# Kernel optimization log

Hardware: AMD Instinct MI355X
Metric: run time of the kernel (lower is better)

Reference implementation:

```python
import jax, jax.numpy as jnp
import numpy as np

QMAX8 = 127.0  # 2**(8-1)-1


def quant1(x, scale):
    # 1-bit symmetric quant: s * sign(x), s = |scale| (per-group mean scale)
    return jnp.abs(scale) * jnp.sign(x)


def quant8(x, scale):
    s = jnp.maximum(jnp.abs(scale), 1e-8)
    q = jnp.clip(jnp.round(x / s), -QMAX8, QMAX8)
    return q * s


def setup_inputs() -> dict:
    key = jax.random.key(0)
    ks = jax.random.split(key, 5)
    p, j, k, m, l, n = 2, 32, 32, 32, 8, 32
    x = jax.random.normal(ks[0], (2, 1024, k * n), dtype=jnp.float32)
    Y_fp = jax.random.normal(ks[1], (p, j, k, m, l), dtype=jnp.float32)
    Z_fp = jax.random.normal(ks[2], (p, j, k, l, n), dtype=jnp.float32)
    A = jax.random.normal(ks[3], (p, j, k, 4), dtype=jnp.float32)
    bias = jax.random.normal(ks[4], (j * m,), dtype=jnp.float32)
    act_scale = jnp.full((1,), 0.001, dtype=jnp.float32)
    return {"x": x, "Y_fp": Y_fp, "Z_fp": Z_fp, "A": A, "bias": bias,
            "act_scale": act_scale}


def reference(x, Y_fp, Z_fp, A, bias, act_scale):
    p, j, k, m, l = Y_fp.shape
    n = Z_fp.shape[-1]
    orig_shape = x.shape[:-1]
    X = x.astype(jnp.float32)
    X = quant8(X, act_scale)  # activation quantization (act_bits=8)

    # per-(p,j,k) mean-abs scales over last two dims
    Y_scale = jnp.mean(jnp.abs(Y_fp), axis=(-2, -1), keepdims=True)
    Z_scale = jnp.mean(jnp.abs(Z_fp), axis=(-2, -1), keepdims=True)
    Y_q = quant1(Y_fp, Y_scale)  # (p,j,k,m,l)
    Z_q = quant1(Z_fp, Z_scale)  # (p,j,k,l,n)

    X_kn = X.reshape(-1, k, n)  # (B,k,n)
    T = jnp.einsum('bkn,pjkln->bpjkl', X_kn, Z_q)
    core = jnp.einsum('pjkml,bpjkl->bpjkm', Y_q, T)

    # quant_bias=True correction terms
    a = A[..., 0][None, ..., None]            # (1,p,j,k,1)
    out1 = jnp.sum(core * a, axis=(1, 3))     # (B,j,m)
    Y_sum = jnp.sum(Y_q, axis=-1)             # (p,j,k,m)
    B_coef = jnp.sum(A[..., 1][..., None] * Y_sum, axis=0)  # (j,k,m)
    Sx = jnp.sum(X_kn, axis=-1)               # (B,k)
    out2 = jnp.einsum('bk,jkm->bjm', Sx, B_coef)
    Zs = jnp.sum(Z_q, axis=-2)                # (p,j,k,n)
    Tz = jnp.einsum('bkn,pjkn->bpjk', X_kn, Zs)
    out3 = jnp.sum(Tz * A[..., 2][None], axis=(1, 3))[..., None]  # (B,j,1)
    D_coef = jnp.sum(A[..., 3], axis=0)       # (j,k)
    out4 = jnp.einsum('bk,jk->bj', Sx, D_coef)[..., None]          # (B,j,1)

    out_bjm = out1 + out2 + out3 + out4       # (B,j,m) via broadcast
    out_2d = out_bjm.reshape(-1, j * m) + bias
    out = out_2d.reshape(*orig_shape, j * m)
    return out.astype(x.dtype)
```

## Files before the change

kernel.cpp:

```cpp
#include <hip/hip_runtime.h>
#include <math.h>
#include <stdint.h>


typedef __attribute__((ext_vector_type(8))) short bf16x8;
typedef __attribute__((ext_vector_type(4))) float f32x4;
typedef __attribute__((ext_vector_type(4))) unsigned short us4;

__device__ __forceinline__ unsigned short f2bf(float f) {
    union { float f; uint32_t u; } c; c.f = f;
    uint32_t r = 0x7fffu + ((c.u >> 16) & 1u);
    return (unsigned short)((c.u + r) >> 16);
}

__device__ __forceinline__ void gl2lds16(const void* g, void* l) {
    __builtin_amdgcn_global_load_lds(
        (const __attribute__((address_space(1))) void*)g,
        (__attribute__((address_space(3))) void*)l, 16, 0, 0);
}

__global__ __launch_bounds__(256) void fused_pre(
    const float* __restrict__ Y,
    const float* __restrict__ Z,
    const float* __restrict__ A,
    const float* __restrict__ x,
    const float* __restrict__ act_scale,
    unsigned short* __restrict__ wt,
    unsigned short* __restrict__ qx)
{
    const int t = threadIdx.x;

    if (blockIdx.x >= 1024) {
        const float s = fmaxf(fabsf(act_scale[0]), 1e-8f);
        const int b2 = blockIdx.x - 1024;
        #pragma unroll
        for (int it = 0; it < 4; ++it) {
            const size_t i4 = (size_t)b2 * 256 + t + (size_t)it * 131072;
            const float4 v = *(const float4*)(x + i4 * 4);
            us4 o;
            o.x = f2bf(fminf(fmaxf(rintf(v.x / s), -127.f), 127.f));
            o.y = f2bf(fminf(fmaxf(rintf(v.y / s), -127.f), 127.f));
            o.z = f2bf(fminf(fmaxf(rintf(v.z / s), -127.f), 127.f));
            o.w = f2bf(fminf(fmaxf(rintf(v.w / s), -127.f), 127.f));
            *(us4*)(qx + i4 * 4) = o;
        }
        return;
    }

    __shared__ unsigned int yb[2][8];
    __shared__ unsigned int zb[2][8];
    __shared__ float wred[16];

    const int jk = blockIdx.x;
    const int jj = jk >> 5;
    const int kk = jk & 31;
    const int n  = t & 31;
    const int mb = t >> 5;
    const int w  = t >> 6;
    const int lane = t & 63;

    const int base0 = jj * 32 + kk;
    const int base1 = 1024 + base0;

    const float yv0 = Y[(size_t)base0 * 256 + t];
    const float yv1 = Y[(size_t)base1 * 256 + t];
    const float zv0 = Z[(size_t)base0 * 256 + t];
    const float zv1 = Z[(size_t)base1 * 256 + t];
    const float a00 = A[(size_t)base0 * 4 + 0], a01 = A[(size_t)base0 * 4 + 1];
    const float a02 = A[(size_t)base0 * 4 + 2], a03 = A[(size_t)base0 * 4 + 3];
    const float a10 = A[(size_t)base1 * 4 + 0], a11 = A[(size_t)base1 * 4 + 1];
    const float a12 = A[(size_t)base1 * 4 + 2], a13 = A[(size_t)base1 * 4 + 3];

    const unsigned long long by0 = __ballot(yv0 < 0.f);
    const unsigned long long by1 = __ballot(yv1 < 0.f);
    const unsigned long long bz0 = __ballot(zv0 < 0.f);
    const unsigned long long bz1 = __ballot(zv1 < 0.f);
    if (lane == 0) {
        yb[0][2 * w] = (unsigned)by0; yb[0][2 * w + 1] = (unsigned)(by0 >> 32);
        yb[1][2 * w] = (unsigned)by1; yb[1][2 * w + 1] = (unsigned)(by1 >> 32);
        zb[0][2 * w] = (unsigned)bz0; zb[0][2 * w + 1] = (unsigned)(bz0 >> 32);
        zb[1][2 * w] = (unsigned)bz1; zb[1][2 * w + 1] = (unsigned)(bz1 >> 32);
    }

    float ay0 = fabsf(yv0), az0 = fabsf(zv0);
    float ay1 = fabsf(yv1), az1 = fabsf(zv1);
    #pragma unroll
    for (int d = 1; d < 64; d <<= 1) {
        ay0 += __shfl_xor(ay0, d, 64);
        az0 += __shfl_xor(az0, d, 64);
        ay1 += __shfl_xor(ay1, d, 64);
        az1 += __shfl_xor(az1, d, 64);
    }
    if (lane == 0) {
        wred[w * 4 + 0] = ay0;
        wred[w * 4 + 1] = az0;
        wred[w * 4 + 2] = ay1;
        wred[w * 4 + 3] = az1;
    }
    __syncthreads();

    const float sY0 = (wred[0] + wred[4] + wred[8]  + wred[12]) * (1.f / 256.f);
    const float sZ0 = (wred[1] + wred[5] + wred[9]  + wred[13]) * (1.f / 256.f);
    const float sY1 = (wred[2] + wred[6] + wred[10] + wred[14]) * (1.f / 256.f);
    const float sZ1 = (wred[3] + wred[7] + wred[11] + wred[15]) * (1.f / 256.f);

    const float c00 = a00 * sY0 * sZ0, c01 = a01 * sY0, c02 = a02 * sZ0;
    const float c10 = a10 * sY1 * sZ1, c11 = a11 * sY1, c12 = a12 * sZ1;
    const float cb  = a03 + a13;

    unsigned sz0 = 0, sz1 = 0;
    #pragma unroll
    for (int l = 0; l < 8; ++l) {
        sz0 |= ((zb[0][l] >> n) & 1u) << l;
        sz1 |= ((zb[1][l] >> n) & 1u) << l;
    }
    const float zc0 = 8.f - 2.f * (float)__popc(sz0);
    const float zc1 = 8.f - 2.f * (float)__popc(sz1);
    const float czc = c02 * zc0 + c12 * zc1 + cb;

    const int ybw = (mb >> 2);
    const int ybs = (mb & 3) * 8;

    #pragma unroll
    for (int q = 0; q < 4; ++q) {
        const int m = mb + 8 * q;
        const unsigned sy0 = (yb[0][2 * q + ybw] >> ybs) & 0xffu;
        const unsigned sy1 = (yb[1][2 * q + ybw] >> ybs) & 0xffu;
        const float w0  = 8.f - 2.f * (float)__popc(sy0 ^ sz0);
        const float w1  = 8.f - 2.f * (float)__popc(sy1 ^ sz1);
        const float ys0 = 8.f - 2.f * (float)__popc(sy0);
        const float ys1 = 8.f - 2.f * (float)__popc(sy1);
        const float acc = c00 * w0 + c01 * ys0 + c10 * w1 + c11 * ys1 + czc;
        wt[(size_t)(jj * 32 + m) * 1024 + kk * 32 + n] = f2bf(acc);
    }
}

__global__ __launch_bounds__(256) void gemm_mfma(
    const unsigned short* __restrict__ qx,
    const unsigned short* __restrict__ wt,
    const float* __restrict__ bias,
    const float* __restrict__ act_scale,
    float* __restrict__ out)
{
    __shared__ __align__(16) short lds[2 * 16384];

    const int tid  = threadIdx.x;
    const int lane = tid & 63;
    const int wave = tid >> 6;
    const int wm = wave >> 1;
    const int wn = wave & 1;
    const int rowBase = blockIdx.y * 64;
    const int colBase = blockIdx.x * 64;

    const float s = fmaxf(fabsf(act_scale[0]), 1e-8f);

    f32x4 acc[2][2];
    #pragma unroll
    for (int i = 0; i < 2; ++i)
        #pragma unroll
        for (int jx = 0; jx < 2; ++jx)
            acc[i][jx] = (f32x4)0.f;

    const int lrow = lane >> 4;
    const int slot = lane & 15;
    const unsigned short* ag[4];
    const unsigned short* bg[4];
    #pragma unroll
    for (int is = 0; is < 4; ++is) {
        const int g   = is * 4 + wave;
        const int row = g * 4 + lrow;
        const int gk  = slot ^ (row & 15);
        ag[is] = qx + (size_t)(rowBase + row) * 1024 + gk * 8;
        bg[is] = wt + (size_t)(colBase + row) * 1024 + gk * 8;
    }

    char* const ldsc = (char*)lds;
    const int q4  = lane >> 4;
    const int l16 = lane & 15;

    #pragma unroll
    for (int is = 0; is < 4; ++is) {
        const int g = is * 4 + wave;
        gl2lds16(ag[is], ldsc + g * 1024);
        gl2lds16(bg[is], ldsc + 16384 + g * 1024);
    }

    for (int kt = 0; kt < 8; ++kt) {
        __syncthreads();

        if (kt + 1 < 8) {
            const int k1 = (kt + 1) * 128;
            char* bb = ldsc + ((kt + 1) & 1) * 32768;
            #pragma unroll
            for (int is = 0; is < 4; ++is) {
                const int g = is * 4 + wave;
                gl2lds16(ag[is] + k1, bb + g * 1024);
                gl2lds16(bg[is] + k1, bb + 16384 + g * 1024);
            }
        }

        const short* As = lds + (kt & 1) * 16384;
        const short* Bs = As + 8192;

        #pragma unroll
        for (int k2 = 0; k2 < 4; ++k2) {
            const int kc = k2 * 4 + q4;
            bf16x8 af[2], bfr[2];
            #pragma unroll
            for (int im = 0; im < 2; ++im) {
                const int r = wm * 32 + im * 16 + l16;
                af[im] = *(const bf16x8*)&As[r * 128 + ((kc ^ (r & 15)) << 3)];
            }
            #pragma unroll
            for (int in = 0; in < 2; ++in) {
                const int r = wn * 32 + in * 16 + l16;
                bfr[in] = *(const bf16x8*)&Bs[r * 128 + ((kc ^ (r & 15)) << 3)];
            }
            #pragma unroll
            for (int im = 0; im < 2; ++im)
                #pragma unroll
                for (int in = 0; in < 2; ++in)
                    acc[im][in] = __builtin_amdgcn_mfma_f32_16x16x32_bf16(
                        af[im], bfr[in], acc[im][in], 0, 0, 0);
        }
    }

    #pragma unroll
    for (int im = 0; im < 2; ++im) {
        #pragma unroll
        for (int in = 0; in < 2; ++in) {
            const int col = colBase + wn * 32 + in * 16 + l16;
            const float b = bias[col];
            #pragma unroll
            for (int r = 0; r < 4; ++r) {
                const int row = rowBase + wm * 32 + im * 16 + q4 * 4 + r;
                out[(size_t)row * 1024 + col] = s * acc[im][in][r] + b;
            }
        }
    }
}

extern "C" void kernel_launch(void* const* d_in, const int* in_sizes, int n_in,
                              void* d_out, int out_size, void* d_ws, size_t ws_size,
                              hipStream_t stream) {
    const float* x         = (const float*)d_in[0];
    const float* Y_fp      = (const float*)d_in[1];
    const float* Z_fp      = (const float*)d_in[2];
    const float* A         = (const float*)d_in[3];
    const float* bias      = (const float*)d_in[4];
    const float* act_scale = (const float*)d_in[5];
    float* out = (float*)d_out;

    unsigned short* wtp = (unsigned short*)d_ws;
    unsigned short* qxp = (unsigned short*)((char*)d_ws + 2 * 1024 * 1024);

    fused_pre<<<dim3(1536), dim3(256), 0, stream>>>(Y_fp, Z_fp, A, x, act_scale, wtp, qxp);
    gemm_mfma<<<dim3(16, 32), dim3(256), 0, stream>>>(qxp, wtp, bias, act_scale, out);
}
```

Before: 81.12 us.

## Fuse preprocessing and GEMM into one cooperative kernel with grid sync

```diff
diff --git a/kernel.cpp b/kernel.cpp
--- a/kernel.cpp
+++ b/kernel.cpp
@@ -1,6 +1,9 @@
 #include <hip/hip_runtime.h>
+#include <hip/hip_cooperative_groups.h>
 #include <math.h>
 #include <stdint.h>
+
+namespace cg = cooperative_groups;
 
 
 typedef __attribute__((ext_vector_type(8))) short bf16x8;
@@ -19,140 +22,149 @@
         (__attribute__((address_space(3))) void*)l, 16, 0, 0);
 }
 
-__global__ __launch_bounds__(256) void fused_pre(
+__global__ __launch_bounds__(256) void fused_all(
+    const float* __restrict__ x,
     const float* __restrict__ Y,
     const float* __restrict__ Z,
     const float* __restrict__ A,
-    const float* __restrict__ x,
+    const float* __restrict__ bias,
     const float* __restrict__ act_scale,
     unsigned short* __restrict__ wt,
-    unsigned short* __restrict__ qx)
-{
-    const int t = threadIdx.x;
-
-    if (blockIdx.x >= 1024) {
-        const float s = fmaxf(fabsf(act_scale[0]), 1e-8f);
-        const int b2 = blockIdx.x - 1024;
-        #pragma unroll
-        for (int it = 0; it < 4; ++it) {
-            const size_t i4 = (size_t)b2 * 256 + t + (size_t)it * 131072;
-            const float4 v = *(const float4*)(x + i4 * 4);
-            us4 o;
-            o.x = f2bf(fminf(fmaxf(rintf(v.x / s), -127.f), 127.f));
-            o.y = f2bf(fminf(fmaxf(rintf(v.y / s), -127.f), 127.f));
-            o.z = f2bf(fminf(fmaxf(rintf(v.z / s), -127.f), 127.f));
-            o.w = f2bf(fminf(fmaxf(rintf(v.w / s), -127.f), 127.f));
-            *(us4*)(qx + i4 * 4) = o;
-        }
-        return;
-    }
-
-    __shared__ unsigned int yb[2][8];
-    __shared__ unsigned int zb[2][8];
-    __shared__ float wred[16];
-
-    const int jk = blockIdx.x;
-    const int jj = jk >> 5;
-    const int kk = jk & 31;
-    const int n  = t & 31;
-    const int mb = t >> 5;
-    const int w  = t >> 6;
-    const int lane = t & 63;
-
-    const int base0 = jj * 32 + kk;
-    const int base1 = 1024 + base0;
-
-    const float yv0 = Y[(size_t)base0 * 256 + t];
-    const float yv1 = Y[(size_t)base1 * 256 + t];
-    const float zv0 = Z[(size_t)base0 * 256 + t];
-    const float zv1 = Z[(size_t)base1 * 256 + t];
-    const float a00 = A[(size_t)base0 * 4 + 0], a01 = A[(size_t)base0 * 4 + 1];
-    const float a02 = A[(size_t)base0 * 4 + 2], a03 = A[(size_t)base0 * 4 + 3];
-    const float a10 = A[(size_t)base1 * 4 + 0], a11 = A[(size_t)base1 * 4 + 1];
-    const float a12 = A[(size_t)base1 * 4 + 2], a13 = A[(size_t)base1 * 4 + 3];
-
-    const unsigned long long by0 = __ballot(yv0 < 0.f);
-    const unsigned long long by1 = __ballot(yv1 < 0.f);
-    const unsigned long long bz0 = __ballot(zv0 < 0.f);
-    const unsigned long long bz1 = __ballot(zv1 < 0.f);
-    if (lane == 0) {
-        yb[0][2 * w] = (unsigned)by0; yb[0][2 * w + 1] = (unsigned)(by0 >> 32);
-        yb[1][2 * w] = (unsigned)by1; yb[1][2 * w + 1] = (unsigned)(by1 >> 32);
-        zb[0][2 * w] = (unsigned)bz0; zb[0][2 * w + 1] = (unsigned)(bz0 >> 32);
-        zb[1][2 * w] = (unsigned)bz1; zb[1][2 * w + 1] = (unsigned)(bz1 >> 32);
-    }
-
-    float ay0 = fabsf(yv0), az0 = fabsf(zv0);
-    float ay1 = fabsf(yv1), az1 = fabsf(zv1);
-    #pragma unroll
-    for (int d = 1; d < 64; d <<= 1) {
-        ay0 += __shfl_xor(ay0, d, 64);
-        az0 += __shfl_xor(az0, d, 64);
-        ay1 += __shfl_xor(ay1, d, 64);
-        az1 += __shfl_xor(az1, d, 64);
-    }
-    if (lane == 0) {
-        wred[w * 4 + 0] = ay0;
-        wred[w * 4 + 1] = az0;
-        wred[w * 4 + 2] = ay1;
-        wred[w * 4 + 3] = az1;
-    }
-    __syncthreads();
-
-    const float sY0 = (wred[0] + wred[4] + wred[8]  + wred[12]) * (1.f / 256.f);
-    const float sZ0 = (wred[1] + wred[5] + wred[9]  + wred[13]) * (1.f / 256.f);
-    const float sY1 = (wred[2] + wred[6] + wred[10] + wred[14]) * (1.f / 256.f);
-    const float sZ1 = (wred[3] + wred[7] + wred[11] + wred[15]) * (1.f / 256.f);
-
-    const float c00 = a00 * sY0 * sZ0, c01 = a01 * sY0, c02 = a02 * sZ0;
-    const float c10 = a10 * sY1 * sZ1, c11 = a11 * sY1, c12 = a12 * sZ1;
-    const float cb  = a03 + a13;
-
-    unsigned sz0 = 0, sz1 = 0;
-    #pragma unroll
-    for (int l = 0; l < 8; ++l) {
-        sz0 |= ((zb[0][l] >> n) & 1u) << l;
-        sz1 |= ((zb[1][l] >> n) & 1u) << l;
-    }
-    const float zc0 = 8.f - 2.f * (float)__popc(sz0);
-    const float zc1 = 8.f - 2.f * (float)__popc(sz1);
-    const float czc = c02 * zc0 + c12 * zc1 + cb;
-
-    const int ybw = (mb >> 2);
-    const int ybs = (mb & 3) * 8;
-
-    #pragma unroll
-    for (int q = 0; q < 4; ++q) {
-        const int m = mb + 8 * q;
-        const unsigned sy0 = (yb[0][2 * q + ybw] >> ybs) & 0xffu;
-        const unsigned sy1 = (yb[1][2 * q + ybw] >> ybs) & 0xffu;
-        const float w0  = 8.f - 2.f * (float)__popc(sy0 ^ sz0);
-        const float w1  = 8.f - 2.f * (float)__popc(sy1 ^ sz1);
-        const float ys0 = 8.f - 2.f * (float)__popc(sy0);
-        const float ys1 = 8.f - 2.f * (float)__popc(sy1);
-        const float acc = c00 * w0 + c01 * ys0 + c10 * w1 + c11 * ys1 + czc;
-        wt[(size_t)(jj * 32 + m) * 1024 + kk * 32 + n] = f2bf(acc);
-    }
-}
-
-__global__ __launch_bounds__(256) void gemm_mfma(
-    const unsigned short* __restrict__ qx,
-    const unsigned short* __restrict__ wt,
-    const float* __restrict__ bias,
-    const float* __restrict__ act_scale,
+    unsigned short* __restrict__ qx,
     float* __restrict__ out)
 {
     __shared__ __align__(16) short lds[2 * 16384];
-
-    const int tid  = threadIdx.x;
-    const int lane = tid & 63;
-    const int wave = tid >> 6;
+    __shared__ unsigned int yb[2][2][8];
+    __shared__ unsigned int zb[2][2][8];
+    __shared__ float wred[2][16];
+
+    const int t    = threadIdx.x;
+    const int lane = t & 63;
+    const int w    = t >> 6;
+    const int bid  = blockIdx.y * 16 + blockIdx.x;
+
+    const float s = fmaxf(fabsf(act_scale[0]), 1e-8f);
+
+    float4 xq[4];
+    #pragma unroll
+    for (int it = 0; it < 4; ++it) {
+        const size_t i4 = (size_t)bid * 256 + t + (size_t)it * 131072;
+        xq[it] = *(const float4*)(x + i4 * 4);
+    }
+
+    const int n  = t & 31;
+    const int mb = t >> 5;
+
+    float yv[2][2], zv[2][2], ac[2][2][4];
+    int jjv[2], kkv[2];
+    #pragma unroll
+    for (int tt = 0; tt < 2; ++tt) {
+        const int jk = bid * 2 + tt;
+        jjv[tt] = jk >> 5;
+        kkv[tt] = jk & 31;
+        #pragma unroll
+        for (int p = 0; p < 2; ++p) {
+            const int base = p * 1024 + jjv[tt] * 32 + kkv[tt];
+            yv[tt][p] = Y[(size_t)base * 256 + t];
+            zv[tt][p] = Z[(size_t)base * 256 + t];
+            ac[tt][p][0] = A[(size_t)base * 4 + 0];
+            ac[tt][p][1] = A[(size_t)base * 4 + 1];
+            ac[tt][p][2] = A[(size_t)base * 4 + 2];
+            ac[tt][p][3] = A[(size_t)base * 4 + 3];
+        }
+    }
+
+    unsigned long long by[2][2], bz[2][2];
+    float ay[2][2], az[2][2];
+    #pragma unroll
+    for (int tt = 0; tt < 2; ++tt)
+        #pragma unroll
+        for (int p = 0; p < 2; ++p) {
+            by[tt][p] = __ballot(yv[tt][p] < 0.f);
+            bz[tt][p] = __ballot(zv[tt][p] < 0.f);
+            ay[tt][p] = fabsf(yv[tt][p]);
+            az[tt][p] = fabsf(zv[tt][p]);
+        }
+    #pragma unroll
+    for (int d = 1; d < 64; d <<= 1)
+        #pragma unroll
+        for (int tt = 0; tt < 2; ++tt)
+            #pragma unroll
+            for (int p = 0; p < 2; ++p) {
+                ay[tt][p] += __shfl_xor(ay[tt][p], d, 64);
+                az[tt][p] += __shfl_xor(az[tt][p], d, 64);
+            }
+    if (lane == 0) {
+        #pragma unroll
+        for (int tt = 0; tt < 2; ++tt)
+            #pragma unroll
+            for (int p = 0; p < 2; ++p) {
+                yb[tt][p][2 * w]     = (unsigned)by[tt][p];
+                yb[tt][p][2 * w + 1] = (unsigned)(by[tt][p] >> 32);
+                zb[tt][p][2 * w]     = (unsigned)bz[tt][p];
+                zb[tt][p][2 * w + 1] = (unsigned)(bz[tt][p] >> 32);
+                wred[tt][w * 4 + p * 2 + 0] = ay[tt][p];
+                wred[tt][w * 4 + p * 2 + 1] = az[tt][p];
+            }
+    }
+    __syncthreads();
+
+    const int ybw = (mb >> 2);
+    const int ybs = (mb & 3) * 8;
+
+    #pragma unroll
+    for (int tt = 0; tt < 2; ++tt) {
+        const float sY0 = (wred[tt][0] + wred[tt][4] + wred[tt][8]  + wred[tt][12]) * (1.f / 256.f);
+        const float sZ0 = (wred[tt][1] + wred[tt][5] + wred[tt][9]  + wred[tt][13]) * (1.f / 256.f);
+        const float sY1 = (wred[tt][2] + wred[tt][6] + wred[tt][10] + wred[tt][14]) * (1.f / 256.f);
+        const float sZ1 = (wred[tt][3] + wred[tt][7] + wred[tt][11] + wred[tt][15]) * (1.f / 256.f);
+
+        const float c00 = ac[tt][0][0] * sY0 * sZ0, c01 = ac[tt][0][1] * sY0, c02 = ac[tt][0][2] * sZ0;
+        const float c10 = ac[tt][1][0] * sY1 * sZ1, c11 = ac[tt][1][1] * sY1, c12 = ac[tt][1][2] * sZ1;
+        const float cb  = ac[tt][0][3] + ac[tt][1][3];
+
+        unsigned sz0 = 0, sz1 = 0;
+        #pragma unroll
+        for (int l = 0; l < 8; ++l) {
+            sz0 |= ((zb[tt][0][l] >> n) & 1u) << l;
+            sz1 |= ((zb[tt][1][l] >> n) & 1u) << l;
+        }
+        const float zc0 = 8.f - 2.f * (float)__popc(sz0);
+        const float zc1 = 8.f - 2.f * (float)__popc(sz1);
+        const float czc = c02 * zc0 + c12 * zc1 + cb;
+
+        #pragma unroll
+        for (int q = 0; q < 4; ++q) {
+            const int m = mb + 8 * q;
+            const unsigned sy0 = (yb[tt][0][2 * q + ybw] >> ybs) & 0xffu;
+            const unsigned sy1 = (yb[tt][1][2 * q + ybw] >> ybs) & 0xffu;
+            const float w0  = 8.f - 2.f * (float)__popc(sy0 ^ sz0);
+            const float w1  = 8.f - 2.f * (float)__popc(sy1 ^ sz1);
+            const float ys0 = 8.f - 2.f * (float)__popc(sy0);
+            const float ys1 = 8.f - 2.f * (float)__popc(sy1);
+            const float accv = c00 * w0 + c01 * ys0 + c10 * w1 + c11 * ys1 + czc;
+            wt[(size_t)(jjv[tt] * 32 + m) * 1024 + kkv[tt] * 32 + n] = f2bf(accv);
+        }
+    }
+
+    #pragma unroll
+    for (int it = 0; it < 4; ++it) {
+        const size_t i4 = (size_t)bid * 256 + t + (size_t)it * 131072;
+        us4 o;
+        o.x = f2bf(fminf(fmaxf(rintf(xq[it].x / s), -127.f), 127.f));
+        o.y = f2bf(fminf(fmaxf(rintf(xq[it].y / s), -127.f), 127.f));
+        o.z = f2bf(fminf(fmaxf(rintf(xq[it].z / s), -127.f), 127.f));
+        o.w = f2bf(fminf(fmaxf(rintf(xq[it].w / s), -127.f), 127.f));
+        *(us4*)(qx + i4 * 4) = o;
+    }
+
+    cg::this_grid().sync();
+
+    const int wave = t >> 6;
     const int wm = wave >> 1;
     const int wn = wave & 1;
     const int rowBase = blockIdx.y * 64;
     const int colBase = blockIdx.x * 64;
-
-    const float s = fmaxf(fabsf(act_scale[0]), 1e-8f);
 
     f32x4 acc[2][2];
     #pragma unroll
@@ -254,6 +266,9 @@
     unsigned short* wtp = (unsigned short*)d_ws;
     unsigned short* qxp = (unsigned short*)((char*)d_ws + 2 * 1024 * 1024);
 
-    fused_pre<<<dim3(1536), dim3(256), 0, stream>>>(Y_fp, Z_fp, A, x, act_scale, wtp, qxp);
-    gemm_mfma<<<dim3(16, 32), dim3(256), 0, stream>>>(qxp, wtp, bias, act_scale, out);
-}
+    void* kargs[] = {(void*)&x, (void*)&Y_fp, (void*)&Z_fp, (void*)&A,
+                     (void*)&bias, (void*)&act_scale,
+                     (void*)&wtp, (void*)&qxp, (void*)&out};
+    hipLaunchCooperativeKernel((const void*)fused_all, dim3(16, 32), dim3(256),
+                               kargs, 0, stream);
+}
```

Measured after the change: 138.7 us. 71.0% more time.

## Fuse activation quantization into GEMM A-tile loading from fp32 input

Applied to the files above, without the earlier changes.

```diff
diff --git a/kernel.cpp b/kernel.cpp
--- a/kernel.cpp
+++ b/kernel.cpp
@@ -19,38 +19,30 @@
         (__attribute__((address_space(3))) void*)l, 16, 0, 0);
 }
 
-__global__ __launch_bounds__(256) void fused_pre(
+__device__ __forceinline__ us4 quant4(float4 v, float invs) {
+    const float q0 = fminf(fmaxf(rintf(v.x * invs), -127.f), 127.f);
+    const float q1 = fminf(fmaxf(rintf(v.y * invs), -127.f), 127.f);
+    const float q2 = fminf(fmaxf(rintf(v.z * invs), -127.f), 127.f);
+    const float q3 = fminf(fmaxf(rintf(v.w * invs), -127.f), 127.f);
+    us4 o;
+    o.x = (unsigned short)(__float_as_uint(q0) >> 16);
+    o.y = (unsigned short)(__float_as_uint(q1) >> 16);
+    o.z = (unsigned short)(__float_as_uint(q2) >> 16);
+    o.w = (unsigned short)(__float_as_uint(q3) >> 16);
+    return o;
+}
+
+__global__ __launch_bounds__(256) void pre_wt(
     const float* __restrict__ Y,
     const float* __restrict__ Z,
     const float* __restrict__ A,
-    const float* __restrict__ x,
-    const float* __restrict__ act_scale,
-    unsigned short* __restrict__ wt,
-    unsigned short* __restrict__ qx)
+    unsigned short* __restrict__ wt)
 {
-    const int t = threadIdx.x;
-
-    if (blockIdx.x >= 1024) {
-        const float s = fmaxf(fabsf(act_scale[0]), 1e-8f);
-        const int b2 = blockIdx.x - 1024;
-        #pragma unroll
-        for (int it = 0; it < 4; ++it) {
-            const size_t i4 = (size_t)b2 * 256 + t + (size_t)it * 131072;
-            const float4 v = *(const float4*)(x + i4 * 4);
-            us4 o;
-            o.x = f2bf(fminf(fmaxf(rintf(v.x / s), -127.f), 127.f));
-            o.y = f2bf(fminf(fmaxf(rintf(v.y / s), -127.f), 127.f));
-            o.z = f2bf(fminf(fmaxf(rintf(v.z / s), -127.f), 127.f));
-            o.w = f2bf(fminf(fmaxf(rintf(v.w / s), -127.f), 127.f));
-            *(us4*)(qx + i4 * 4) = o;
-        }
-        return;
-    }
-
     __shared__ unsigned int yb[2][8];
     __shared__ unsigned int zb[2][8];
     __shared__ float wred[16];
 
+    const int t  = threadIdx.x;
     const int jk = blockIdx.x;
     const int jj = jk >> 5;
     const int kk = jk & 31;
@@ -136,7 +128,7 @@
 }
 
 __global__ __launch_bounds__(256) void gemm_mfma(
-    const unsigned short* __restrict__ qx,
+    const float* __restrict__ x,
     const unsigned short* __restrict__ wt,
     const float* __restrict__ bias,
     const float* __restrict__ act_scale,
@@ -153,6 +145,7 @@
     const int colBase = blockIdx.x * 64;
 
     const float s = fmaxf(fabsf(act_scale[0]), 1e-8f);
+    const float invs = 1.0f / s;
 
     f32x4 acc[2][2];
     #pragma unroll
@@ -161,16 +154,19 @@
         for (int jx = 0; jx < 2; ++jx)
             acc[i][jx] = (f32x4)0.f;
 
+    const int rw0  = tid >> 5;
+    const int sc   = (tid & 31) >> 1;
+    const int off4 = (tid & 1) * 4;
+    const float* xg = x + (size_t)(rowBase + rw0) * 1024 + (tid & 31) * 4;
+
     const int lrow = lane >> 4;
     const int slot = lane & 15;
-    const unsigned short* ag[4];
     const unsigned short* bg[4];
     #pragma unroll
     for (int is = 0; is < 4; ++is) {
         const int g   = is * 4 + wave;
         const int row = g * 4 + lrow;
         const int gk  = slot ^ (row & 15);
-        ag[is] = qx + (size_t)(rowBase + row) * 1024 + gk * 8;
         bg[is] = wt + (size_t)(colBase + row) * 1024 + gk * 8;
     }
 
@@ -178,24 +174,41 @@
     const int q4  = lane >> 4;
     const int l16 = lane & 15;
 
-    #pragma unroll
-    for (int is = 0; is < 4; ++is) {
-        const int g = is * 4 + wave;
-        gl2lds16(ag[is], ldsc + g * 1024);
-        gl2lds16(bg[is], ldsc + 16384 + g * 1024);
-    }
+    float4 xf[8];
+    #pragma unroll
+    for (int i = 0; i < 8; ++i) xf[i] = *(const float4*)(xg + (size_t)i * 8192);
+    #pragma unroll
+    for (int i = 0; i < 8; ++i) {
+        const us4 aq = quant4(xf[i], invs);
+        const int r = 8 * i + rw0;
+        *(us4*)&lds[(r * 16 + (sc ^ (r & 15))) * 8 + off4] = aq;
+    }
+    #pragma unroll
+    for (int is = 0; is < 4; ++is)
+        gl2lds16(bg[is], ldsc + 16384 + (is * 4 + wave) * 1024);
+    #pragma unroll
+    for (int i = 0; i < 8; ++i)
+        xf[i] = *(const float4*)(xg + 128 + (size_t)i * 8192);
 
     for (int kt = 0; kt < 8; ++kt) {
         __syncthreads();
 
         if (kt + 1 < 8) {
-            const int k1 = (kt + 1) * 128;
             char* bb = ldsc + ((kt + 1) & 1) * 32768;
             #pragma unroll
-            for (int is = 0; is < 4; ++is) {
-                const int g = is * 4 + wave;
-                gl2lds16(ag[is] + k1, bb + g * 1024);
-                gl2lds16(bg[is] + k1, bb + 16384 + g * 1024);
+            for (int is = 0; is < 4; ++is)
+                gl2lds16(bg[is] + (kt + 1) * 128, bb + 16384 + (is * 4 + wave) * 1024);
+            short* ab = lds + ((kt + 1) & 1) * 16384;
+            #pragma unroll
+            for (int i = 0; i < 8; ++i) {
+                const us4 aq = quant4(xf[i], invs);
+                const int r = 8 * i + rw0;
+                *(us4*)&ab[(r * 16 + (sc ^ (r & 15))) * 8 + off4] = aq;
+            }
+            if (kt + 2 < 8) {
+                #pragma unroll
+                for (int i = 0; i < 8; ++i)
+                    xf[i] = *(const float4*)(xg + (kt + 2) * 128 + (size_t)i * 8192);
             }
         }
 
@@ -252,8 +265,7 @@
     float* out = (float*)d_out;
 
     unsigned short* wtp = (unsigned short*)d_ws;
-    unsigned short* qxp = (unsigned short*)((char*)d_ws + 2 * 1024 * 1024);
-
-    fused_pre<<<dim3(1536), dim3(256), 0, stream>>>(Y_fp, Z_fp, A, x, act_scale, wtp, qxp);
-    gemm_mfma<<<dim3(16, 32), dim3(256), 0, stream>>>(qxp, wtp, bias, act_scale, out);
-}
+
+    pre_wt<<<dim3(1024), dim3(256), 0, stream>>>(Y_fp, Z_fp, A, wtp);
+    gemm_mfma<<<dim3(16, 32), dim3(256), 0, stream>>>(x, wtp, bias, act_scale, out);
+}
```

Result: slower. 86.41 us (+6.5%).
